# Kernel optimization log

Measured on AMD Instinct MI355X. Metric: run time of the kernel, lower is better.

Reference implementation:

```python
import jax, jax.numpy as jnp
import numpy as np

B, S, L = 8, 2048, 8
H, NH = 768, 12
DH = H // NH
NUM_REL = 100
LN_EPS = 1e-5


def setup_inputs() -> dict:
    key = jax.random.key(0)
    ks = jax.random.split(key, 16)
    inp = {
        'text_embeddings': jax.random.normal(ks[0], (B, S, H), dtype=jnp.float32),
        # values in [-1, 64); -1 marks 'no leaf' and is masked out
        'graph_structure': jax.random.randint(ks[1], (B, S, L), -1, 64, dtype=jnp.int64),
        'relation_ids': jax.random.randint(ks[2], (B, S, L), 0, NUM_REL, dtype=jnp.int64),
        'rel_table': jax.random.normal(ks[3], (NUM_REL, H), dtype=jnp.float32),
        'Wq': jax.random.normal(ks[4], (H, H), dtype=jnp.float32) / np.sqrt(H),
        'bq': jnp.zeros((H,), dtype=jnp.float32),
        'Wk': jax.random.normal(ks[5], (H, H), dtype=jnp.float32) / np.sqrt(H),
        'bk': jnp.zeros((H,), dtype=jnp.float32),
        'Wv': jax.random.normal(ks[6], (H, H), dtype=jnp.float32) / np.sqrt(H),
        'bv': jnp.zeros((H,), dtype=jnp.float32),
        'Wo': jax.random.normal(ks[7], (H, H), dtype=jnp.float32) / np.sqrt(H),
        'bo': jnp.zeros((H,), dtype=jnp.float32),
        'gamma': jnp.ones((H,), dtype=jnp.float32),
        'beta': jnp.zeros((H,), dtype=jnp.float32),
    }
    return inp


def reference(text_embeddings, graph_structure, relation_ids, rel_table,
              Wq, bq, Wk, bk, Wv, bv, Wo, bo, gamma, beta):
    b, s, h = text_embeddings.shape
    l = relation_ids.shape[2]
    # embedding gather (clamp -1 -> 0, masked later)
    rel_emb = rel_table[jnp.clip(relation_ids, 0, None)]  # [B,S,L,H]
    # projections; query has length-1 per root token
    q = (text_embeddings @ Wq + bq).reshape(b, s, NH, DH)          # [B,S,N,D]
    k = (rel_emb @ Wk + bk).reshape(b, s, l, NH, DH)               # [B,S,L,N,D]
    v = (rel_emb @ Wv + bv).reshape(b, s, l, NH, DH)
    scores = jnp.einsum('bsnd,bslnd->bsnl', q, k) / np.sqrt(DH)    # [B,S,N,L]
    mask = (graph_structure != -1)[:, :, None, :]                  # [B,S,1,L]
    scores = jnp.where(mask, scores, jnp.float32(-10000.0))
    probs = jax.nn.softmax(scores, axis=-1)                        # [B,S,N,L]
    ctx = jnp.einsum('bsnl,bslnd->bsnd', probs, v).reshape(b, s, h)
    out = ctx @ Wo + bo
    x = text_embeddings + out
    mu = jnp.mean(x, axis=-1, keepdims=True)
    var = jnp.mean(jnp.square(x - mu), axis=-1, keepdims=True)
    return (x - mu) * jax.lax.rsqrt(var + LN_EPS) * gamma + beta
```

## Files before the change

kernel.cpp:

```cpp
#include <hip/hip_runtime.h>
#include <hip/hip_bf16.h>

#define H 768
#define NH 12
#define DH 64
#define LL 8
#define NTOK 16384
#define NREL 100
#define NRELP 128
#define PADW 72

typedef __attribute__((ext_vector_type(8))) short short8;
typedef __attribute__((ext_vector_type(4))) float f32x4;

__device__ __forceinline__ float bf2f(ushort u) {
  union { unsigned int i; float f; } v; v.i = ((unsigned int)u) << 16; return v.f;
}
__device__ __forceinline__ float bflo(unsigned int u) {
  union { unsigned int i; float f; } v; v.i = u << 16; return v.f;
}
__device__ __forceinline__ float bfhi(unsigned int u) {
  union { unsigned int i; float f; } v; v.i = u & 0xffff0000u; return v.f;
}
__device__ __forceinline__ ushort f2bf(float f) {
  union { float f; unsigned int i; } v; v.f = f;
  unsigned int x = v.i;
  return (ushort)((x + 0x7fffu + ((x >> 16) & 1u)) >> 16);
}
__device__ __forceinline__ unsigned int cvt_pk_bf16(float lo, float hi) {
  unsigned int r;
  asm("v_cvt_pk_bf16_f32 %0, %1, %2" : "=v"(r) : "v"(lo), "v"(hi));
  return r;
}

__global__ __launch_bounds__(256) void prep_kernel(
    const float* __restrict__ s0, ushort* __restrict__ d0,
    const float* __restrict__ s1, ushort* __restrict__ d1,
    const float* __restrict__ s2, ushort* __restrict__ d2,
    const float* __restrict__ s3, ushort* __restrict__ d3,
    const float* __restrict__ rel, ushort* __restrict__ RelB) {
  if (blockIdx.z == 4) {
    int b = blockIdx.y * 24 + blockIdx.x;
    if (b < 96) {
      int i = (b * 256 + threadIdx.x) * 4;
      int row = i / H;
      ushort4 o = {0, 0, 0, 0};
      if (row < NREL) {
        float4 v = *(const float4*)(rel + i);
        o.x = f2bf(v.x); o.y = f2bf(v.y); o.z = f2bf(v.z); o.w = f2bf(v.w);
      }
      *(ushort4*)(RelB + i) = o;
    }
    return;
  }
  const float* src; ushort* dst;
  switch (blockIdx.z) {
    case 0:  src = s0; dst = d0; break;
    case 1:  src = s1; dst = d1; break;
    case 2:  src = s2; dst = d2; break;
    default: src = s3; dst = d3; break;
  }
  __shared__ float tile[32][33];
  int bx = blockIdx.x * 32, by = blockIdx.y * 32;
  int tx = threadIdx.x & 31, ty = threadIdx.x >> 5;
  #pragma unroll
  for (int i = 0; i < 32; i += 8)
    tile[ty + i][tx] = src[(size_t)(by + ty + i) * H + bx + tx];
  __syncthreads();
  #pragma unroll
  for (int i = 0; i < 32; i += 8)
    dst[(size_t)(bx + ty + i) * H + by + tx] = f2bf(tile[tx][ty + i]);
}

__device__ __forceinline__ void gload_lds16(const void* g, void* l) {
  __builtin_amdgcn_global_load_lds(
      (const __attribute__((address_space(1))) unsigned int*)g,
      (__attribute__((address_space(3))) unsigned int*)l, 16, 0, 0);
}

#define BM 128
#define BN 128
#define BK 64

#define GEMM_COMPUTE_EPILOGUE()                                                \
  __syncthreads();                                                             \
  _Pragma("unroll")                                                            \
  for (int kk = 0; kk < 2; ++kk) {                                             \
    const int sw = (((kk << 2) | lk) ^ (lr & 7)) * 8;                          \
    short8 af[4], bfr[4];                                                      \
    _Pragma("unroll")                                                          \
    for (int m = 0; m < 4; ++m)                                                \
      af[m] = *(const short8*)(As + (wr * 64 + m * 16 + lr) * BK + sw);        \
    _Pragma("unroll")                                                          \
    for (int n = 0; n < 4; ++n)                                                \
      bfr[n] = *(const short8*)(Bs + (wc * 64 + n * 16 + lr) * BK + sw);       \
    _Pragma("unroll")                                                          \
    for (int m = 0; m < 4; ++m)                                                \
      _Pragma("unroll")                                                        \
      for (int n = 0; n < 4; ++n)                                              \
        acc[m][n] = __builtin_amdgcn_mfma_f32_16x16x32_bf16(af[m], bfr[n],     \
                                                            acc[m][n], 0, 0, 0);\
  }                                                                            \
  __syncthreads();

__device__ __forceinline__ void gemm_body(
    ushort* As, ushort* Bs,
    const ushort* __restrict__ A,
    const ushort* __restrict__ Bt,
    const float* __restrict__ bias,
    ushort* __restrict__ C,
    int M, int N, int K, int bx, int by) {
  const int tid = threadIdx.x;
  const int row0 = by * BM;
  const int col0 = bx * BN;
  const int wave = tid >> 6;
  const int lane = tid & 63;
  const int wr = wave >> 1, wc = wave & 1;
  const int lr = lane & 15, lk = lane >> 4;
  f32x4 acc[4][4];
  #pragma unroll
  for (int m = 0; m < 4; ++m)
    #pragma unroll
    for (int n = 0; n < 4; ++n) acc[m][n] = (f32x4)(0.f);

  for (int k0 = 0; k0 < K; k0 += BK) {
    #pragma unroll
    for (int i = 0; i < 4; ++i) {
      int c = tid + i * 256;
      int r = c >> 3, s = c & 7;
      int gs = s ^ (r & 7);
      gload_lds16(A  + (size_t)(row0 + r) * K + k0 + gs * 8, (char*)As + c * 16);
      gload_lds16(Bt + (size_t)(col0 + r) * K + k0 + gs * 8, (char*)Bs + c * 16);
    }
    GEMM_COMPUTE_EPILOGUE()
  }
  #pragma unroll
  for (int m = 0; m < 4; ++m) {
    #pragma unroll
    for (int n = 0; n < 4; ++n) {
      int col = col0 + wc * 64 + n * 16 + lr;
      float b = bias[col];
      #pragma unroll
      for (int j = 0; j < 4; ++j) {
        int row = row0 + wr * 64 + m * 16 + lk * 4 + j;
        C[(size_t)row * N + col] = f2bf(acc[m][n][j] + b);
      }
    }
  }
}

__device__ __forceinline__ void gemm_body_a32(
    ushort* As, ushort* Bs,
    const float* __restrict__ A32,
    const ushort* __restrict__ Bt,
    const float* __restrict__ bias,
    ushort* __restrict__ C,
    int M, int N, int K, int bx, int by) {
  const int tid = threadIdx.x;
  const int row0 = by * BM;
  const int col0 = bx * BN;
  const int wave = tid >> 6;
  const int lane = tid & 63;
  const int wr = wave >> 1, wc = wave & 1;
  const int lr = lane & 15, lk = lane >> 4;
  f32x4 acc[4][4];
  #pragma unroll
  for (int m = 0; m < 4; ++m)
    #pragma unroll
    for (int n = 0; n < 4; ++n) acc[m][n] = (f32x4)(0.f);

  for (int k0 = 0; k0 < K; k0 += BK) {
    #pragma unroll
    for (int i = 0; i < 4; ++i) {
      int c = tid + i * 256;
      int r = c >> 3, s = c & 7;
      int gs = s ^ (r & 7);
      gload_lds16(Bt + (size_t)(col0 + r) * K + k0 + gs * 8, (char*)Bs + c * 16);
      const float* src = A32 + (size_t)(row0 + r) * K + k0 + gs * 8;
      float4 f0 = *(const float4*)(src);
      float4 f1 = *(const float4*)(src + 4);
      uint4 w;
      w.x = cvt_pk_bf16(f0.x, f0.y);
      w.y = cvt_pk_bf16(f0.z, f0.w);
      w.z = cvt_pk_bf16(f1.x, f1.y);
      w.w = cvt_pk_bf16(f1.z, f1.w);
      *(uint4*)((char*)As + c * 16) = w;
    }
    GEMM_COMPUTE_EPILOGUE()
  }
  #pragma unroll
  for (int m = 0; m < 4; ++m) {
    #pragma unroll
    for (int n = 0; n < 4; ++n) {
      int col = col0 + wc * 64 + n * 16 + lr;
      float b = bias[col];
      #pragma unroll
      for (int j = 0; j < 4; ++j) {
        int row = row0 + wr * 64 + m * 16 + lk * 4 + j;
        C[(size_t)row * N + col] = f2bf(acc[m][n][j] + b);
      }
    }
  }
}

__global__ __launch_bounds__(256, 2) void gemm_q_kv_kernel(
    const float* __restrict__ X, const ushort* __restrict__ WqT,
    const float* __restrict__ bq, ushort* __restrict__ Qbf,
    const ushort* __restrict__ RelB,
    const ushort* __restrict__ WkT, const float* __restrict__ bk, ushort* __restrict__ Ktab,
    const ushort* __restrict__ WvT, const float* __restrict__ bv, ushort* __restrict__ Vtab) {
  __shared__ ushort As[BM * BK];
  __shared__ ushort Bs[BN * BK];
  int lin = blockIdx.x;
  if (lin < 12) {
    if (lin < 6) gemm_body(As, Bs, RelB, WkT, bk, Ktab, NRELP, H, H, lin, 0);
    else         gemm_body(As, Bs, RelB, WvT, bv, Vtab, NRELP, H, H, lin - 6, 0);
    return;
  }
  int l2 = lin - 12;
  int wg = (l2 & 7) * 96 + (l2 >> 3);
  gemm_body_a32(As, Bs, X, WqT, bq, Qbf, NTOK, H, H, wg % 6, wg / 6);
}

__global__ __launch_bounds__(256, 2) void gemm_bt_kernel(
    const ushort* __restrict__ A, const ushort* __restrict__ Bt,
    const float* __restrict__ bias, ushort* __restrict__ C,
    int M, int N, int K) {
  __shared__ ushort As[BM * BK];
  __shared__ ushort Bs[BN * BK];
  int lin = blockIdx.y * gridDim.x + blockIdx.x;
  int q = (gridDim.x * gridDim.y) >> 3;
  int wg = (lin & 7) * q + (lin >> 3);
  gemm_body(As, Bs, A, Bt, bias, C, M, N, K, wg % gridDim.x, wg / gridDim.x);
}

__global__ __launch_bounds__(256) void attn3_kernel(
    const ushort* __restrict__ Q,
    const ushort* __restrict__ Ktab,
    const ushort* __restrict__ Vtab,
    const int* __restrict__ graph,
    const int* __restrict__ relid,
    ushort* __restrict__ Ctx) {
  __shared__ __align__(16) ushort Ks[NREL * PADW];
  __shared__ __align__(16) ushort Vs[NREL * PADW];
  const int tid = threadIdx.x;
  const int head = blockIdx.y;
  const int t = blockIdx.x * 256 + tid;

  #pragma unroll
  for (int i = 0; i < 4; ++i) {
    int c = tid + i * 256;
    if (c < NREL * 9) {
      int row = c / 9, slot = c - row * 9;
      int gs = (slot < 8) ? slot * 8 : 0;
      const size_t src = (size_t)row * H + head * DH + gs;
      gload_lds16(Ktab + src, (char*)Ks + (size_t)c * 16);
      gload_lds16(Vtab + src, (char*)Vs + (size_t)c * 16);
    }
  }

  const uint4* qp = (const uint4*)(Q + (size_t)t * H + head * DH);
  uint4 qw[8];
  #pragma unroll
  for (int j = 0; j < 8; ++j) qw[j] = qp[j];
  const int4* gp = (const int4*)(graph + (size_t)t * LL);
  const int4* rp = (const int4*)(relid + (size_t)t * LL);
  int4 ga = gp[0], gb = gp[1];
  int4 ra = rp[0], rb = rp[1];
  int gs[8] = {ga.x, ga.y, ga.z, ga.w, gb.x, gb.y, gb.z, gb.w};
  int rid[8] = {ra.x, ra.y, ra.z, ra.w, rb.x, rb.y, rb.z, rb.w};
  int koff[8];
  #pragma unroll
  for (int l = 0; l < 8; ++l) {
    int r = rid[l] < 0 ? 0 : rid[l];
    koff[l] = r * (PADW * 2);
  }

  __syncthreads();

  float s[8];
  #pragma unroll
  for (int l = 0; l < 8; ++l) s[l] = 0.f;
  #pragma unroll
  for (int j = 0; j < 8; ++j) {
    float qf[8];
    qf[0] = bflo(qw[j].x); qf[1] = bfhi(qw[j].x);
    qf[2] = bflo(qw[j].y); qf[3] = bfhi(qw[j].y);
    qf[4] = bflo(qw[j].z); qf[5] = bfhi(qw[j].z);
    qf[6] = bflo(qw[j].w); qf[7] = bfhi(qw[j].w);
    #pragma unroll
    for (int l = 0; l < 8; ++l) {
      uint4 kw = *(const uint4*)((const char*)Ks + koff[l] + j * 16);
      s[l] += qf[0] * bflo(kw.x) + qf[1] * bfhi(kw.x)
            + qf[2] * bflo(kw.y) + qf[3] * bfhi(kw.y)
            + qf[4] * bflo(kw.z) + qf[5] * bfhi(kw.z)
            + qf[6] * bflo(kw.w) + qf[7] * bfhi(kw.w);
    }
  }

  #pragma unroll
  for (int l = 0; l < 8; ++l)
    s[l] = (gs[l] != -1) ? s[l] * 0.125f : -10000.0f;
  float mx = s[0];
  #pragma unroll
  for (int l = 1; l < 8; ++l) mx = fmaxf(mx, s[l]);
  float p[8], den = 0.f;
  #pragma unroll
  for (int l = 0; l < 8; ++l) { p[l] = __expf(s[l] - mx); den += p[l]; }
  float inv = 1.f / den;
  #pragma unroll
  for (int l = 0; l < 8; ++l) p[l] *= inv;

  ushort* cp = Ctx + (size_t)t * H + head * DH;
  #pragma unroll
  for (int j = 0; j < 8; ++j) {
    float a[8];
    #pragma unroll
    for (int d = 0; d < 8; ++d) a[d] = 0.f;
    #pragma unroll
    for (int l = 0; l < 8; ++l) {
      uint4 vw = *(const uint4*)((const char*)Vs + koff[l] + j * 16);
      a[0] += p[l] * bflo(vw.x); a[1] += p[l] * bfhi(vw.x);
      a[2] += p[l] * bflo(vw.y); a[3] += p[l] * bfhi(vw.y);
      a[4] += p[l] * bflo(vw.z); a[5] += p[l] * bfhi(vw.z);
      a[6] += p[l] * bflo(vw.w); a[7] += p[l] * bfhi(vw.w);
    }
    short8 o;
    #pragma unroll
    for (int d = 0; d < 8; ++d) o[d] = (short)f2bf(a[d]);
    *(short8*)(cp + j * 8) = o;
  }
}

__global__ __launch_bounds__(192) void ln_kernel(
    const float* __restrict__ text, const ushort* __restrict__ op,
    const float* __restrict__ gamma, const float* __restrict__ beta,
    float* __restrict__ out) {
  int t = blockIdx.x;
  int c0 = threadIdx.x * 4;
  float4 tv = *(const float4*)(text + (size_t)t * H + c0);
  ushort4 ov = *(const ushort4*)(op + (size_t)t * H + c0);
  float x0 = tv.x + bf2f(ov.x), x1 = tv.y + bf2f(ov.y);
  float x2 = tv.z + bf2f(ov.z), x3 = tv.w + bf2f(ov.w);
  float s = x0 + x1 + x2 + x3;
  float s2 = x0 * x0 + x1 * x1 + x2 * x2 + x3 * x3;
  #pragma unroll
  for (int off = 32; off > 0; off >>= 1) {
    s  += __shfl_xor(s, off, 64);
    s2 += __shfl_xor(s2, off, 64);
  }
  __shared__ float red[2][3];
  int wave = threadIdx.x >> 6, lane = threadIdx.x & 63;
  if (lane == 0) { red[0][wave] = s; red[1][wave] = s2; }
  __syncthreads();
  s  = red[0][0] + red[0][1] + red[0][2];
  s2 = red[1][0] + red[1][1] + red[1][2];
  float mu = s * (1.f / H);
  float var = s2 * (1.f / H) - mu * mu;
  float rs = rsqrtf(var + 1e-5f);
  float4 g4 = *(const float4*)(gamma + c0);
  float4 b4 = *(const float4*)(beta + c0);
  float4 o4;
  o4.x = (x0 - mu) * rs * g4.x + b4.x;
  o4.y = (x1 - mu) * rs * g4.y + b4.y;
  o4.z = (x2 - mu) * rs * g4.z + b4.z;
  o4.w = (x3 - mu) * rs * g4.w + b4.w;
  *(float4*)(out + (size_t)t * H + c0) = o4;
}

extern "C" void kernel_launch(void* const* d_in, const int* in_sizes, int n_in,
                              void* d_out, int out_size, void* d_ws, size_t ws_size,
                              hipStream_t stream) {
  const float* text      = (const float*)d_in[0];
  const int*   graph     = (const int*)d_in[1];
  const int*   relid     = (const int*)d_in[2];
  const float* rel_table = (const float*)d_in[3];
  const float* Wq = (const float*)d_in[4];  const float* bq = (const float*)d_in[5];
  const float* Wk = (const float*)d_in[6];  const float* bk = (const float*)d_in[7];
  const float* Wv = (const float*)d_in[8];  const float* bv = (const float*)d_in[9];
  const float* Wo = (const float*)d_in[10]; const float* bo = (const float*)d_in[11];
  const float* gamma = (const float*)d_in[12];
  const float* beta  = (const float*)d_in[13];
  float* out = (float*)d_out;
  char* ws = (char*)d_ws;

  const size_t TOKH = (size_t)NTOK * H;
  size_t off = 0;
  ushort* Ctx  = (ushort*)(ws + off); off += TOKH * 2;
  ushort* Qbf  = (ushort*)(ws + off); off += TOKH * 2;
  ushort* WqT  = (ushort*)(ws + off); off += (size_t)H * H * 2;
  ushort* WoT  = (ushort*)(ws + off); off += (size_t)H * H * 2;
  ushort* WkT  = (ushort*)(ws + off); off += (size_t)H * H * 2;
  ushort* WvT  = (ushort*)(ws + off); off += (size_t)H * H * 2;
  ushort* RelB = (ushort*)(ws + off); off += (size_t)NRELP * H * 2;
  ushort* Ktab = (ushort*)(ws + off); off += (size_t)NRELP * H * 2;
  ushort* Vtab = (ushort*)(ws + off); off += (size_t)NRELP * H * 2;

  prep_kernel<<<dim3(24, 24, 5), 256, 0, stream>>>(
      Wq, WqT, Wo, WoT, Wk, WkT, Wv, WvT, rel_table, RelB);
  gemm_q_kv_kernel<<<780, 256, 0, stream>>>(
      text, WqT, bq, Qbf, RelB, WkT, bk, Ktab, WvT, bv, Vtab);
  dim3 ga(NTOK / 256, NH);
  attn3_kernel<<<ga, 256, 0, stream>>>(Qbf, Ktab, Vtab, graph, relid, Ctx);
  dim3 g1(H / BN, NTOK / BM);
  gemm_bt_kernel<<<g1, 256, 0, stream>>>(Ctx, WoT, bo, Qbf, NTOK, H, H);
  ln_kernel<<<NTOK, 192, 0, stream>>>(text, Qbf, gamma, beta, out);
}
```

Before: 109.7 us.

## Double-buffer LDS tiles in GEMM kernels to overlap loads with MFMA

Gives both GEMM bodies two LDS buffers for A and B. The next K-tile is prefetched while MFMAs run on the current one, which leaves one barrier per iteration instead of two. In the fp32-A variant, the global loads are issued into registers before compute and converted to bf16 and stored to LDS afterward. LDS use doubles to 64KB per block, and the extra registers could hurt occupancy under launch_bounds(256,2).

```diff
diff --git a/kernel.cpp b/kernel.cpp
--- a/kernel.cpp
+++ b/kernel.cpp
@@ -81,27 +81,41 @@
 #define BM 128
 #define BN 128
 #define BK 64
-
-#define GEMM_COMPUTE_EPILOGUE()                                                \
-  __syncthreads();                                                             \
+#define TILE (BM * BK)
+
+#define GEMM_COMPUTE(cb)                                                       \
   _Pragma("unroll")                                                            \
   for (int kk = 0; kk < 2; ++kk) {                                             \
     const int sw = (((kk << 2) | lk) ^ (lr & 7)) * 8;                          \
     short8 af[4], bfr[4];                                                      \
     _Pragma("unroll")                                                          \
     for (int m = 0; m < 4; ++m)                                                \
-      af[m] = *(const short8*)(As + (wr * 64 + m * 16 + lr) * BK + sw);        \
+      af[m] = *(const short8*)(As + (cb) * TILE + (wr * 64 + m * 16 + lr) * BK + sw); \
     _Pragma("unroll")                                                          \
     for (int n = 0; n < 4; ++n)                                                \
-      bfr[n] = *(const short8*)(Bs + (wc * 64 + n * 16 + lr) * BK + sw);       \
+      bfr[n] = *(const short8*)(Bs + (cb) * TILE + (wc * 64 + n * 16 + lr) * BK + sw); \
     _Pragma("unroll")                                                          \
     for (int m = 0; m < 4; ++m)                                                \
       _Pragma("unroll")                                                        \
       for (int n = 0; n < 4; ++n)                                              \
         acc[m][n] = __builtin_amdgcn_mfma_f32_16x16x32_bf16(af[m], bfr[n],     \
                                                             acc[m][n], 0, 0, 0);\
-  }                                                                            \
-  __syncthreads();
+  }
+
+#define GEMM_EPILOGUE()                                                        \
+  _Pragma("unroll")                                                            \
+  for (int m = 0; m < 4; ++m) {                                                \
+    _Pragma("unroll")                                                          \
+    for (int n = 0; n < 4; ++n) {                                              \
+      int col = col0 + wc * 64 + n * 16 + lr;                                  \
+      float b = bias[col];                                                     \
+      _Pragma("unroll")                                                        \
+      for (int j = 0; j < 4; ++j) {                                            \
+        int row = row0 + wr * 64 + m * 16 + lk * 4 + j;                        \
+        C[(size_t)row * N + col] = f2bf(acc[m][n][j] + b);                     \
+      }                                                                        \
+    }                                                                          \
+  }
 
 __device__ __forceinline__ void gemm_body(
     ushort* As, ushort* Bs,
@@ -123,30 +137,36 @@
     #pragma unroll
     for (int n = 0; n < 4; ++n) acc[m][n] = (f32x4)(0.f);
 
-  for (int k0 = 0; k0 < K; k0 += BK) {
-    #pragma unroll
-    for (int i = 0; i < 4; ++i) {
-      int c = tid + i * 256;
-      int r = c >> 3, s = c & 7;
-      int gs = s ^ (r & 7);
-      gload_lds16(A  + (size_t)(row0 + r) * K + k0 + gs * 8, (char*)As + c * 16);
-      gload_lds16(Bt + (size_t)(col0 + r) * K + k0 + gs * 8, (char*)Bs + c * 16);
-    }
-    GEMM_COMPUTE_EPILOGUE()
-  }
-  #pragma unroll
-  for (int m = 0; m < 4; ++m) {
-    #pragma unroll
-    for (int n = 0; n < 4; ++n) {
-      int col = col0 + wc * 64 + n * 16 + lr;
-      float b = bias[col];
+  const int nt = K / BK;
+  #pragma unroll
+  for (int i = 0; i < 4; ++i) {
+    int c = tid + i * 256;
+    int r = c >> 3, s = c & 7;
+    int gs = s ^ (r & 7);
+    gload_lds16(A  + (size_t)(row0 + r) * K + gs * 8, (char*)As + c * 16);
+    gload_lds16(Bt + (size_t)(col0 + r) * K + gs * 8, (char*)Bs + c * 16);
+  }
+  __syncthreads();
+  int cb = 0;
+  for (int t = 0; t < nt; ++t) {
+    if (t + 1 < nt) {
+      int k0 = (t + 1) * BK;
       #pragma unroll
-      for (int j = 0; j < 4; ++j) {
-        int row = row0 + wr * 64 + m * 16 + lk * 4 + j;
-        C[(size_t)row * N + col] = f2bf(acc[m][n][j] + b);
+      for (int i = 0; i < 4; ++i) {
+        int c = tid + i * 256;
+        int r = c >> 3, s = c & 7;
+        int gs = s ^ (r & 7);
+        gload_lds16(A  + (size_t)(row0 + r) * K + k0 + gs * 8,
+                    (char*)As + (cb ^ 1) * (TILE * 2) + c * 16);
+        gload_lds16(Bt + (size_t)(col0 + r) * K + k0 + gs * 8,
+                    (char*)Bs + (cb ^ 1) * (TILE * 2) + c * 16);
       }
     }
-  }
+    GEMM_COMPUTE(cb)
+    __syncthreads();
+    cb ^= 1;
+  }
+  GEMM_EPILOGUE()
 }
 
 __device__ __forceinline__ void gemm_body_a32(
@@ -169,38 +189,58 @@
     #pragma unroll
     for (int n = 0; n < 4; ++n) acc[m][n] = (f32x4)(0.f);
 
-  for (int k0 = 0; k0 < K; k0 += BK) {
-    #pragma unroll
-    for (int i = 0; i < 4; ++i) {
-      int c = tid + i * 256;
-      int r = c >> 3, s = c & 7;
-      int gs = s ^ (r & 7);
-      gload_lds16(Bt + (size_t)(col0 + r) * K + k0 + gs * 8, (char*)Bs + c * 16);
-      const float* src = A32 + (size_t)(row0 + r) * K + k0 + gs * 8;
-      float4 f0 = *(const float4*)(src);
-      float4 f1 = *(const float4*)(src + 4);
-      uint4 w;
-      w.x = cvt_pk_bf16(f0.x, f0.y);
-      w.y = cvt_pk_bf16(f0.z, f0.w);
-      w.z = cvt_pk_bf16(f1.x, f1.y);
-      w.w = cvt_pk_bf16(f1.z, f1.w);
-      *(uint4*)((char*)As + c * 16) = w;
-    }
-    GEMM_COMPUTE_EPILOGUE()
-  }
-  #pragma unroll
-  for (int m = 0; m < 4; ++m) {
-    #pragma unroll
-    for (int n = 0; n < 4; ++n) {
-      int col = col0 + wc * 64 + n * 16 + lr;
-      float b = bias[col];
+  const int nt = K / BK;
+  #pragma unroll
+  for (int i = 0; i < 4; ++i) {
+    int c = tid + i * 256;
+    int r = c >> 3, s = c & 7;
+    int gs = s ^ (r & 7);
+    gload_lds16(Bt + (size_t)(col0 + r) * K + gs * 8, (char*)Bs + c * 16);
+    const float* src = A32 + (size_t)(row0 + r) * K + gs * 8;
+    float4 f0 = *(const float4*)(src);
+    float4 f1 = *(const float4*)(src + 4);
+    uint4 w;
+    w.x = cvt_pk_bf16(f0.x, f0.y);
+    w.y = cvt_pk_bf16(f0.z, f0.w);
+    w.z = cvt_pk_bf16(f1.x, f1.y);
+    w.w = cvt_pk_bf16(f1.z, f1.w);
+    *(uint4*)((char*)As + c * 16) = w;
+  }
+  __syncthreads();
+  int cb = 0;
+  for (int t = 0; t < nt; ++t) {
+    float4 fa[4][2];
+    if (t + 1 < nt) {
+      int k0 = (t + 1) * BK;
       #pragma unroll
-      for (int j = 0; j < 4; ++j) {
-        int row = row0 + wr * 64 + m * 16 + lk * 4 + j;
-        C[(size_t)row * N + col] = f2bf(acc[m][n][j] + b);
+      for (int i = 0; i < 4; ++i) {
+        int c = tid + i * 256;
+        int r = c >> 3, s = c & 7;
+        int gs = s ^ (r & 7);
+        gload_lds16(Bt + (size_t)(col0 + r) * K + k0 + gs * 8,
+                    (char*)Bs + (cb ^ 1) * (TILE * 2) + c * 16);
+        const float* src = A32 + (size_t)(row0 + r) * K + k0 + gs * 8;
+        fa[i][0] = *(const float4*)(src);
+        fa[i][1] = *(const float4*)(src + 4);
       }
     }
-  }
+    GEMM_COMPUTE(cb)
+    if (t + 1 < nt) {
+      #pragma unroll
+      for (int i = 0; i < 4; ++i) {
+        int c = tid + i * 256;
+        uint4 w;
+        w.x = cvt_pk_bf16(fa[i][0].x, fa[i][0].y);
+        w.y = cvt_pk_bf16(fa[i][0].z, fa[i][0].w);
+        w.z = cvt_pk_bf16(fa[i][1].x, fa[i][1].y);
+        w.w = cvt_pk_bf16(fa[i][1].z, fa[i][1].w);
+        *(uint4*)((char*)As + (cb ^ 1) * (TILE * 2) + c * 16) = w;
+      }
+    }
+    __syncthreads();
+    cb ^= 1;
+  }
+  GEMM_EPILOGUE()
 }
 
 __global__ __launch_bounds__(256, 2) void gemm_q_kv_kernel(
@@ -209,29 +249,29 @@
     const ushort* __restrict__ RelB,
     const ushort* __restrict__ WkT, const float* __restrict__ bk, ushort* __restrict__ Ktab,
     const ushort* __restrict__ WvT, const float* __restrict__ bv, ushort* __restrict__ Vtab) {
-  __shared__ ushort As[BM * BK];
-  __shared__ ushort Bs[BN * BK];
+  __shared__ ushort As[2][TILE];
+  __shared__ ushort Bs[2][TILE];
   int lin = blockIdx.x;
   if (lin < 12) {
-    if (lin < 6) gemm_body(As, Bs, RelB, WkT, bk, Ktab, NRELP, H, H, lin, 0);
-    else         gemm_body(As, Bs, RelB, WvT, bv, Vtab, NRELP, H, H, lin - 6, 0);
+    if (lin < 6) gemm_body(&As[0][0], &Bs[0][0], RelB, WkT, bk, Ktab, NRELP, H, H, lin, 0);
+    else         gemm_body(&As[0][0], &Bs[0][0], RelB, WvT, bv, Vtab, NRELP, H, H, lin - 6, 0);
     return;
   }
   int l2 = lin - 12;
   int wg = (l2 & 7) * 96 + (l2 >> 3);
-  gemm_body_a32(As, Bs, X, WqT, bq, Qbf, NTOK, H, H, wg % 6, wg / 6);
+  gemm_body_a32(&As[0][0], &Bs[0][0], X, WqT, bq, Qbf, NTOK, H, H, wg % 6, wg / 6);
 }
 
 __global__ __launch_bounds__(256, 2) void gemm_bt_kernel(
     const ushort* __restrict__ A, const ushort* __restrict__ Bt,
     const float* __restrict__ bias, ushort* __restrict__ C,
     int M, int N, int K) {
-  __shared__ ushort As[BM * BK];
-  __shared__ ushort Bs[BN * BK];
+  __shared__ ushort As[2][TILE];
+  __shared__ ushort Bs[2][TILE];
   int lin = blockIdx.y * gridDim.x + blockIdx.x;
   int q = (gridDim.x * gridDim.y) >> 3;
   int wg = (lin & 7) * q + (lin >> 3);
-  gemm_body(As, Bs, A, Bt, bias, C, M, N, K, wg % gridDim.x, wg / gridDim.x);
+  gemm_body(&As[0][0], &Bs[0][0], A, Bt, bias, C, M, N, K, wg % gridDim.x, wg / gridDim.x);
 }
 
 __global__ __launch_bounds__(256) void attn3_kernel(
```

New measurement: 124.8 us. 1.14x slower.
